# Optimization experiments

Measured on AMD Instinct MI355X. Metric: run time of the kernel, lower is better.

## Reference

```python
import jax, jax.numpy as jnp
import numpy as np

N_NODES = 100000
N_EDGES = 1600000
C = 64


def _spline_conv(x, src, dst, u, w, root, bias, n_nodes):
    """SplineConv, dim=1, kernel_size=2, degree=1, open spline, aggr='mean'.

    For K=2, degree=1, pseudo u in [0,1]: basis = (1-u) on knot 0, u on knot 1.
    message_e = (1-u_e) * x[src_e] @ w[0] + u_e * x[src_e] @ w[1]
    Compute the two GEMMs at node level (N < E) then gather, which is
    mathematically identical and cheaper.
    """
    h0 = x @ w[0]  # [N, C]
    h1 = x @ w[1]  # [N, C]
    uc = u[:, None]  # [E, 1]
    msg = (1.0 - uc) * h0[src] + uc * h1[src]  # [E, C]
    agg = jax.ops.segment_sum(msg, dst, num_segments=n_nodes)  # [N, C]
    deg = jax.ops.segment_sum(jnp.ones_like(u), dst, num_segments=n_nodes)
    agg = agg / jnp.maximum(deg, 1.0)[:, None]  # mean aggregation
    return agg + x @ root + bias


def setup_inputs() -> dict:
    key = jax.random.key(0)
    ks = jax.random.split(key, 10)
    x = jax.random.normal(ks[0], (N_NODES, C), dtype=jnp.float32)
    edge_index = jax.random.randint(ks[1], (2, N_EDGES), 0, N_NODES, dtype=jnp.int64)
    edge_attr = jax.random.uniform(ks[2], (N_EDGES, 1), dtype=jnp.float32)
    s = 1.0 / np.sqrt(C)
    w1 = jax.random.uniform(ks[3], (2, C, C), jnp.float32, -s, s)
    root1 = jax.random.uniform(ks[4], (C, C), jnp.float32, -s, s)
    b1 = jnp.zeros((C,), jnp.float32)
    w2 = jax.random.uniform(ks[5], (2, C, C), jnp.float32, -s, s)
    root2 = jax.random.uniform(ks[6], (C, C), jnp.float32, -s, s)
    b2 = jnp.zeros((C,), jnp.float32)
    return {"x": x, "edge_index": edge_index, "edge_attr": edge_attr,
            "w1": w1, "root1": root1, "b1": b1,
            "w2": w2, "root2": root2, "b2": b2}


def reference(x, edge_index, edge_attr, w1, root1, b1, w2, root2, b2):
    src, dst = edge_index[0], edge_index[1]
    u = edge_attr[:, 0]
    n = x.shape[0]
    h = _spline_conv(x, src, dst, u, w1, root1, b1, n)
    h = _spline_conv(h, src, dst, u, w2, root2, b2, n)
    return h
```

## Files before the change

### kernel.cpp

```cpp
#include <hip/hip_runtime.h>

#define CDIM 64

typedef __attribute__((ext_vector_type(8))) short bf16x8;
typedef __attribute__((ext_vector_type(4))) float f32x4;

__device__ __forceinline__ short bf16r(float f) {
    unsigned a = __float_as_uint(f);
    a = (a + 0x7fffu + ((a >> 16) & 1u)) >> 16;
    return (short)a;
}
__device__ __forceinline__ unsigned bfpack(float lo, float hi) {
    unsigned a = __float_as_uint(lo);
    a = (a + 0x7fffu + ((a >> 16) & 1u)) >> 16;
    unsigned b = __float_as_uint(hi);
    b = (b + 0x7fffu + ((b >> 16) & 1u)) & 0xffff0000u;
    return a | b;
}

#define NPB_SHIFT 9
#define BKN (1 << NPB_SHIFT)
#define BPAD 10240
#define PART_CH 2048
#define RCAP 1536

__global__ __launch_bounds__(256) void k_build(
        const int* __restrict__ src, const int* __restrict__ dst,
        const float* __restrict__ u, int* __restrict__ bkt_cursor,
        unsigned long long* __restrict__ rec, int n_edges, int n_buckets, int gP,
        const float* __restrict__ x, unsigned* __restrict__ xb32, size_t n2,
        const float* __restrict__ w1, const float* __restrict__ root1,
        const float* __restrict__ w2, const float* __restrict__ root2,
        short* __restrict__ wtg) {
    __shared__ int cnt_s[256];
    __shared__ int excl_s[256];
    __shared__ int cur_s[256];
    __shared__ int goff_s[256];
    __shared__ int tot_s;
    __shared__ unsigned long long rec_s[PART_CH];
    __shared__ int tgt_s[PART_CH];
    int tid = threadIdx.x;
    int bid = blockIdx.x;

    if (bid >= gP) {
        int r = bid - gP;
        if (r < 2) {
            const float* s0 = r ? w2 : w1;
            const float* srcs[3] = {s0, s0 + 4096, r ? root2 : root1};
            short* o = wtg + (size_t)r * 3 * 4096;
            for (int i = tid; i < 12288; i += 256) {
                int m = i >> 12, rr = i & 4095, k = rr >> 6, n = rr & 63;
                o[(m << 12) + (n << 6) + k] = bf16r(srcs[m][rr]);
            }
        } else {
            size_t t = (size_t)(r - 2) * 256 + tid;
            size_t stride = (size_t)(gridDim.x - gP - 2) * 256;
            for (size_t i = t; i < n2; i += stride) {
                float2 v = ((const float2*)x)[i];
                xb32[i] = bfpack(v.x, v.y);
            }
        }
        return;
    }

    cnt_s[tid] = 0;
    __syncthreads();
    int e0 = bid * PART_CH + tid * 8;
    int d[8], s[8];
    float uu[8];
    if (e0 + 8 <= n_edges) {
        int4 d0 = *(const int4*)(dst + e0), d1 = *(const int4*)(dst + e0 + 4);
        int4 s0 = *(const int4*)(src + e0), s1 = *(const int4*)(src + e0 + 4);
        float4 u0 = *(const float4*)(u + e0), u1 = *(const float4*)(u + e0 + 4);
        d[0]=d0.x; d[1]=d0.y; d[2]=d0.z; d[3]=d0.w; d[4]=d1.x; d[5]=d1.y; d[6]=d1.z; d[7]=d1.w;
        s[0]=s0.x; s[1]=s0.y; s[2]=s0.z; s[3]=s0.w; s[4]=s1.x; s[5]=s1.y; s[6]=s1.z; s[7]=s1.w;
        uu[0]=u0.x; uu[1]=u0.y; uu[2]=u0.z; uu[3]=u0.w; uu[4]=u1.x; uu[5]=u1.y; uu[6]=u1.z; uu[7]=u1.w;
    } else {
#pragma unroll
        for (int i = 0; i < 8; ++i) {
            int e = e0 + i;
            bool ok = e < n_edges;
            d[i] = ok ? dst[e] : -1;
            s[i] = ok ? src[e] : 0;
            uu[i] = ok ? u[e] : 0.f;
        }
    }
#pragma unroll
    for (int i = 0; i < 8; ++i)
        if (d[i] >= 0) atomicAdd(&cnt_s[d[i] >> NPB_SHIFT], 1);
    __syncthreads();
    int c = cnt_s[tid];
    excl_s[tid] = c;
    __syncthreads();
    for (int off = 1; off < 256; off <<= 1) {
        int t = (tid >= off) ? excl_s[tid - off] : 0;
        __syncthreads();
        excl_s[tid] += t;
        __syncthreads();
    }
    int excl = excl_s[tid] - c;
    if (tid == 255) tot_s = excl_s[255];
    __syncthreads();
    excl_s[tid] = excl;
    cur_s[tid] = excl;
    goff_s[tid] = 0;
    if (tid < n_buckets && c) goff_s[tid] = tid * BPAD + atomicAdd(&bkt_cursor[tid], c);
    __syncthreads();
#pragma unroll
    for (int i = 0; i < 8; ++i) {
        if (d[i] >= 0) {
            int b = d[i] >> NPB_SHIFT;
            int p = atomicAdd(&cur_s[b], 1);
            unsigned uq = (unsigned)(uu[i] * 32767.0f + 0.5f);
            rec_s[p] = ((unsigned long long)(unsigned)d[i] << 32)
                     | (unsigned long long)(((unsigned)s[i] << 15) | uq);
            tgt_s[p] = goff_s[b] + (p - excl_s[b]);
        }
    }
    __syncthreads();
    int tot = tot_s;
    for (int i = tid; i < tot; i += 256)
        rec[tgt_s[i]] = rec_s[i];
}

__global__ __launch_bounds__(512) void k_fused(
        const unsigned* __restrict__ xb_in,
        const unsigned long long* __restrict__ rec,
        const int* __restrict__ bkt_cursor,
        const short* __restrict__ wb,
        const float* __restrict__ bias,
        float* __restrict__ out,
        unsigned short* __restrict__ xb_out,
        unsigned* __restrict__ em_g,
        unsigned* __restrict__ rowcnt_g,
        int n_nodes, int n_buckets, int build) {
    __shared__ unsigned em_s[RCAP];
    __shared__ unsigned tmp_em[RCAP];
    __shared__ unsigned short tmp_d[RCAP];
    __shared__ int cnt_s[64];
    __shared__ int row_s[64];
    __shared__ int cur_s[64];
    __shared__ int nm_s;
    __shared__ __align__(16) unsigned gl[64][68];
    int tid = threadIdx.x;
    int blk = blockIdx.x;
    int b = (blk & 7) + 8 * (blk >> 6);
    int sub = (blk >> 3) & 7;
    if (b >= n_buckets) return;
    int lo = (b << NPB_SHIFT) + (sub << 6);
    int region = ((b << 3) + sub) * RCAP;
    const float inv15 = 1.0f / 32767.0f;

    if (build) {
        int nrec = bkt_cursor[b];
        const unsigned long long* r0 = rec + (size_t)b * BPAD;
        if (tid < 64) cnt_s[tid] = 0;
        if (tid == 0) nm_s = 0;
        __syncthreads();
        for (int i = tid; i < nrec; i += 512) {
            unsigned long long r = r0[i];
            int rel = (int)(r >> 32) - lo;
            if ((unsigned)rel < 64u) {
                int p = atomicAdd(&nm_s, 1);
                if (p < RCAP) {
                    tmp_em[p] = (unsigned)r;
                    tmp_d[p] = (unsigned short)rel;
                    atomicAdd(&cnt_s[rel], 1);
                }
            }
        }
        __syncthreads();
        if (tid < 64) row_s[tid] = cnt_s[tid];
        __syncthreads();
        for (int off = 1; off < 64; off <<= 1) {
            int t = (tid < 64 && tid >= off) ? row_s[tid - off] : 0;
            __syncthreads();
            if (tid < 64) row_s[tid] += t;
            __syncthreads();
        }
        if (tid < 64) {
            row_s[tid] -= cnt_s[tid];
            cur_s[tid] = row_s[tid];
        }
        __syncthreads();
        int nm = min(nm_s, RCAP);
        for (int i = tid; i < nm; i += 512) {
            int rel = tmp_d[i];
            int p = atomicAdd(&cur_s[rel], 1);
            em_s[p] = tmp_em[i];
        }
        __syncthreads();
        if (tid < 64)
            rowcnt_g[((b << 3) + sub) * 64 + tid] =
                (unsigned)row_s[tid] | ((unsigned)cnt_s[tid] << 16);
        for (int i = tid; i < nm; i += 512) em_g[region + i] = em_s[i];
    } else {
        if (tid < 64) {
            unsigned rc = rowcnt_g[((b << 3) + sub) * 64 + tid];
            row_s[tid] = (int)(rc & 0xffffu);
            cnt_s[tid] = (int)(rc >> 16);
        }
        __syncthreads();
    }

    const unsigned* em = build ? (const unsigned*)&em_s[0] : (em_g + region);
    int qid = tid >> 4;
    int ql = tid & 15;
    for (int t = 0; t < 2; ++t) {
        int rel = qid * 2 + t;
        int start = row_s[rel];
        int cnt = cnt_s[rel];
        int end = start + cnt;
        float a0 = 0.f, a1 = 0.f, a2 = 0.f, a3 = 0.f;
        float b0 = 0.f, b1 = 0.f, b2 = 0.f, b3 = 0.f;
        int j = start;
        for (; j + 4 <= end; j += 4) {
            unsigned e[4]; uint2 v[4];
#pragma unroll
            for (int i = 0; i < 4; ++i) e[i] = em[j + i];
#pragma unroll
            for (int i = 0; i < 4; ++i)
                v[i] = *(const uint2*)(xb_in + (size_t)(e[i] >> 15) * 32 + 2 * ql);
#pragma unroll
            for (int i = 0; i < 4; ++i) {
                float uu = (float)(e[i] & 0x7fffu) * inv15;
                float wa = 1.0f - uu;
                float c0 = __uint_as_float(v[i].x << 16);
                float c1 = __uint_as_float(v[i].x & 0xffff0000u);
                float c2 = __uint_as_float(v[i].y << 16);
                float c3 = __uint_as_float(v[i].y & 0xffff0000u);
                a0 += wa * c0; a1 += wa * c1; a2 += wa * c2; a3 += wa * c3;
                b0 += uu * c0; b1 += uu * c1; b2 += uu * c2; b3 += uu * c3;
            }
        }
        if (j < end) {
            unsigned e[4]; uint2 v[4]; float m[4];
#pragma unroll
            for (int i = 0; i < 4; ++i) {
                int idx = j + i;
                bool ok = idx < end;
                e[i] = em[ok ? idx : (end - 1)];
                m[i] = ok ? 1.0f : 0.0f;
            }
#pragma unroll
            for (int i = 0; i < 4; ++i)
                v[i] = *(const uint2*)(xb_in + (size_t)(e[i] >> 15) * 32 + 2 * ql);
#pragma unroll
            for (int i = 0; i < 4; ++i) {
                float uu = (float)(e[i] & 0x7fffu) * inv15;
                float wa = (1.0f - uu) * m[i], wu = uu * m[i];
                float c0 = __uint_as_float(v[i].x << 16);
                float c1 = __uint_as_float(v[i].x & 0xffff0000u);
                float c2 = __uint_as_float(v[i].y << 16);
                float c3 = __uint_as_float(v[i].y & 0xffff0000u);
                a0 += wa * c0; a1 += wa * c1; a2 += wa * c2; a3 += wa * c3;
                b0 += wu * c0; b1 += wu * c1; b2 += wu * c2; b3 += wu * c3;
            }
        }
        float s = 1.0f / fmaxf((float)cnt, 1.0f);
        *(uint2*)&gl[rel][2 * ql] = make_uint2(bfpack(a0 * s, a1 * s), bfpack(a2 * s, a3 * s));
        *(uint2*)&gl[rel][32 + 2 * ql] = make_uint2(bfpack(b0 * s, b1 * s), bfpack(b2 * s, b3 * s));
    }
    __syncthreads();

    int wv = tid >> 6;
    int lane = tid & 63;
    int tile = wv & 3;
    int nthalf = wv >> 2;
    int quad = lane >> 4;
    int m16 = lane & 15;
    int rown = tile * 16 + m16;
    int arow = lo + rown;
    bool rowok = arow < n_nodes;
    const short* gp = (const short*)&gl[rown][0];
    const unsigned* xp = xb_in + (size_t)arow * 32;
    bf16x8 zf = {0, 0, 0, 0, 0, 0, 0, 0};
    bf16x8 aG0[2], aG1[2], aX[2];
#pragma unroll
    for (int kf = 0; kf < 2; ++kf) {
        aG0[kf] = *(const bf16x8*)(gp + kf * 32 + quad * 8);
        aG1[kf] = *(const bf16x8*)(gp + 64 + kf * 32 + quad * 8);
        aX[kf] = rowok ? *(const bf16x8*)(xp + kf * 16 + quad * 4) : zf;
    }
#pragma unroll
    for (int nh = 0; nh < 2; ++nh) {
        int nt = nthalf * 2 + nh;
        f32x4 accv = {0.f, 0.f, 0.f, 0.f};
#pragma unroll
        for (int kf = 0; kf < 2; ++kf) {
            int col = nt * 16 + m16;
            bf16x8 bw0 = *(const bf16x8*)(wb + (col << 6) + kf * 32 + quad * 8);
            bf16x8 bw1 = *(const bf16x8*)(wb + ((64 + col) << 6) + kf * 32 + quad * 8);
            bf16x8 bwR = *(const bf16x8*)(wb + ((128 + col) << 6) + kf * 32 + quad * 8);
            accv = __builtin_amdgcn_mfma_f32_16x16x32_bf16(aG0[kf], bw0, accv, 0, 0, 0);
            accv = __builtin_amdgcn_mfma_f32_16x16x32_bf16(aG1[kf], bw1, accv, 0, 0, 0);
            accv = __builtin_amdgcn_mfma_f32_16x16x32_bf16(aX[kf], bwR, accv, 0, 0, 0);
        }
        float bcol = bias[nt * 16 + m16];
#pragma unroll
        for (int r = 0; r < 4; ++r) {
            int node = lo + tile * 16 + quad * 4 + r;
            if (node < n_nodes) {
                size_t off = (size_t)node * CDIM + nt * 16 + m16;
                float o = accv[r] + bcol;
                if (out) out[off] = o;
                if (xb_out) xb_out[off] = (unsigned short)bf16r(o);
            }
        }
    }
}

extern "C" void kernel_launch(void* const* d_in, const int* in_sizes, int n_in,
                              void* d_out, int out_size, void* d_ws, size_t ws_size,
                              hipStream_t stream) {
    const float* x = (const float*)d_in[0];
    const int* edge_index = (const int*)d_in[1];
    const float* edge_attr = (const float*)d_in[2];
    const float* w1 = (const float*)d_in[3];
    const float* root1 = (const float*)d_in[4];
    const float* b1 = (const float*)d_in[5];
    const float* w2 = (const float*)d_in[6];
    const float* root2 = (const float*)d_in[7];
    const float* b2 = (const float*)d_in[8];

    int n_nodes = in_sizes[0] / CDIM;
    int n_edges = in_sizes[2];
    const int* src = edge_index;
    const int* dst = edge_index + n_edges;

    size_t F = (size_t)n_nodes * CDIM;
    int n_buckets = (n_nodes + BKN - 1) >> NPB_SHIFT;
    int nb8 = n_buckets * 8;
    unsigned* xbA = (unsigned*)d_ws;
    unsigned* xbB = xbA + F / 2;
    int* bkt_cursor = (int*)(xbB + F / 2);
    uintptr_t p = (uintptr_t)(bkt_cursor + n_buckets);
    p = (p + 15) & ~(uintptr_t)15;
    short* wtg = (short*)p;
    p += (size_t)2 * 3 * 4096 * sizeof(short);
    p = (p + 15) & ~(uintptr_t)15;
    unsigned* em_g = (unsigned*)p;
    p += (size_t)nb8 * RCAP * sizeof(unsigned);
    unsigned* rowcnt_g = (unsigned*)p;
    p += (size_t)nb8 * 64 * sizeof(unsigned);
    p = (p + 15) & ~(uintptr_t)15;
    unsigned long long* rec = (unsigned long long*)p;
    float* out = (float*)d_out;

    int gP = (n_edges + PART_CH - 1) / PART_CH;
    int gB = gP + 2 + 2048;
    int gF = 64 * ((n_buckets + 7) / 8);

    hipMemsetAsync(bkt_cursor, 0, n_buckets * sizeof(int), stream);
    k_build<<<gB, 256, 0, stream>>>(src, dst, edge_attr, bkt_cursor, rec,
                                    n_edges, n_buckets, gP,
                                    x, xbA, F / 2, w1, root1, w2, root2, wtg);

    k_fused<<<gF, 512, 0, stream>>>(xbA, rec, bkt_cursor, wtg, b1,
                                    nullptr, (unsigned short*)xbB,
                                    em_g, rowcnt_g, n_nodes, n_buckets, 1);
    k_fused<<<gF, 512, 0, stream>>>(xbB, rec, bkt_cursor, wtg + 3 * 4096, b2,
                                    out, nullptr,
                                    em_g, rowcnt_g, n_nodes, n_buckets, 0);
}
```

Measured before the change: 257.7 us.

## Split fused kernel into specialized build and second-layer gather kernels

The single k_fused kernel is split into a build-specialized version for layer one and a lean k_go kernel for layer two. k_go uses 256-thread blocks with no build scratch in shared memory and only the 64x68 staging tile, so more blocks can be resident per CU during the gather-heavy second pass. It also uses a simpler linear block-to-node mapping. Bucket cursors are padded to separate cache lines to reduce atomic contention in k_build. The cost is extra code, and the padding makes the memset slightly larger.

Result: faster. 251.3 us (-2.5%).

```diff
diff --git a/kernel.cpp b/kernel.cpp
--- a/kernel.cpp
+++ b/kernel.cpp
@@ -23,6 +23,7 @@
 #define BPAD 10240
 #define PART_CH 2048
 #define RCAP 1536
+#define CPAD 16
 
 __global__ __launch_bounds__(256) void k_build(
         const int* __restrict__ src, const int* __restrict__ dst,
@@ -104,7 +105,8 @@
     excl_s[tid] = excl;
     cur_s[tid] = excl;
     goff_s[tid] = 0;
-    if (tid < n_buckets && c) goff_s[tid] = tid * BPAD + atomicAdd(&bkt_cursor[tid], c);
+    if (tid < n_buckets && c)
+        goff_s[tid] = tid * BPAD + atomicAdd(&bkt_cursor[tid * CPAD], c);
     __syncthreads();
 #pragma unroll
     for (int i = 0; i < 8; ++i) {
@@ -123,17 +125,16 @@
         rec[tgt_s[i]] = rec_s[i];
 }
 
-__global__ __launch_bounds__(512) void k_fused(
+__global__ __launch_bounds__(512) void k_fused_build(
         const unsigned* __restrict__ xb_in,
         const unsigned long long* __restrict__ rec,
         const int* __restrict__ bkt_cursor,
         const short* __restrict__ wb,
         const float* __restrict__ bias,
-        float* __restrict__ out,
         unsigned short* __restrict__ xb_out,
         unsigned* __restrict__ em_g,
         unsigned* __restrict__ rowcnt_g,
-        int n_nodes, int n_buckets, int build) {
+        int n_nodes, int n_buckets) {
     __shared__ unsigned em_s[RCAP];
     __shared__ unsigned tmp_em[RCAP];
     __shared__ unsigned short tmp_d[RCAP];
@@ -151,59 +152,49 @@
     int region = ((b << 3) + sub) * RCAP;
     const float inv15 = 1.0f / 32767.0f;
 
-    if (build) {
-        int nrec = bkt_cursor[b];
-        const unsigned long long* r0 = rec + (size_t)b * BPAD;
-        if (tid < 64) cnt_s[tid] = 0;
-        if (tid == 0) nm_s = 0;
+    int nrec = bkt_cursor[b * CPAD];
+    const unsigned long long* r0 = rec + (size_t)b * BPAD;
+    if (tid < 64) cnt_s[tid] = 0;
+    if (tid == 0) nm_s = 0;
+    __syncthreads();
+    for (int i = tid; i < nrec; i += 512) {
+        unsigned long long r = r0[i];
+        int rel = (int)(r >> 32) - lo;
+        if ((unsigned)rel < 64u) {
+            int p = atomicAdd(&nm_s, 1);
+            if (p < RCAP) {
+                tmp_em[p] = (unsigned)r;
+                tmp_d[p] = (unsigned short)rel;
+                atomicAdd(&cnt_s[rel], 1);
+            }
+        }
+    }
+    __syncthreads();
+    if (tid < 64) row_s[tid] = cnt_s[tid];
+    __syncthreads();
+    for (int off = 1; off < 64; off <<= 1) {
+        int t = (tid < 64 && tid >= off) ? row_s[tid - off] : 0;
         __syncthreads();
-        for (int i = tid; i < nrec; i += 512) {
-            unsigned long long r = r0[i];
-            int rel = (int)(r >> 32) - lo;
-            if ((unsigned)rel < 64u) {
-                int p = atomicAdd(&nm_s, 1);
-                if (p < RCAP) {
-                    tmp_em[p] = (unsigned)r;
-                    tmp_d[p] = (unsigned short)rel;
-                    atomicAdd(&cnt_s[rel], 1);
-                }
-            }
-        }
+        if (tid < 64) row_s[tid] += t;
         __syncthreads();
-        if (tid < 64) row_s[tid] = cnt_s[tid];
-        __syncthreads();
-        for (int off = 1; off < 64; off <<= 1) {
-            int t = (tid < 64 && tid >= off) ? row_s[tid - off] : 0;
-            __syncthreads();
-            if (tid < 64) row_s[tid] += t;
-            __syncthreads();
-        }
-        if (tid < 64) {
-            row_s[tid] -= cnt_s[tid];
-            cur_s[tid] = row_s[tid];
-        }
-        __syncthreads();
-        int nm = min(nm_s, RCAP);
-        for (int i = tid; i < nm; i += 512) {
-            int rel = tmp_d[i];
-            int p = atomicAdd(&cur_s[rel], 1);
-            em_s[p] = tmp_em[i];
-        }
-        __syncthreads();
-        if (tid < 64)
-            rowcnt_g[((b << 3) + sub) * 64 + tid] =
-                (unsigned)row_s[tid] | ((unsigned)cnt_s[tid] << 16);
-        for (int i = tid; i < nm; i += 512) em_g[region + i] = em_s[i];
-    } else {
-        if (tid < 64) {
-            unsigned rc = rowcnt_g[((b << 3) + sub) * 64 + tid];
-            row_s[tid] = (int)(rc & 0xffffu);
-            cnt_s[tid] = (int)(rc >> 16);
-        }
-        __syncthreads();
-    }
-
-    const unsigned* em = build ? (const unsigned*)&em_s[0] : (em_g + region);
+    }
+    if (tid < 64) {
+        row_s[tid] -= cnt_s[tid];
+        cur_s[tid] = row_s[tid];
+    }
+    __syncthreads();
+    int nm = min(nm_s, RCAP);
+    for (int i = tid; i < nm; i += 512) {
+        int rel = tmp_d[i];
+        int p = atomicAdd(&cur_s[rel], 1);
+        em_s[p] = tmp_em[i];
+    }
+    __syncthreads();
+    if (tid < 64)
+        rowcnt_g[((b << 3) + sub) * 64 + tid] =
+            (unsigned)row_s[tid] | ((unsigned)cnt_s[tid] << 16);
+    for (int i = tid; i < nm; i += 512) em_g[region + i] = em_s[i];
+
     int qid = tid >> 4;
     int ql = tid & 15;
     for (int t = 0; t < 2; ++t) {
@@ -217,7 +208,7 @@
         for (; j + 4 <= end; j += 4) {
             unsigned e[4]; uint2 v[4];
 #pragma unroll
-            for (int i = 0; i < 4; ++i) e[i] = em[j + i];
+            for (int i = 0; i < 4; ++i) e[i] = em_s[j + i];
 #pragma unroll
             for (int i = 0; i < 4; ++i)
                 v[i] = *(const uint2*)(xb_in + (size_t)(e[i] >> 15) * 32 + 2 * ql);
@@ -239,7 +230,7 @@
             for (int i = 0; i < 4; ++i) {
                 int idx = j + i;
                 bool ok = idx < end;
-                e[i] = em[ok ? idx : (end - 1)];
+                e[i] = em_s[ok ? idx : (end - 1)];
                 m[i] = ok ? 1.0f : 0.0f;
             }
 #pragma unroll
@@ -302,9 +293,123 @@
             int node = lo + tile * 16 + quad * 4 + r;
             if (node < n_nodes) {
                 size_t off = (size_t)node * CDIM + nt * 16 + m16;
-                float o = accv[r] + bcol;
-                if (out) out[off] = o;
-                if (xb_out) xb_out[off] = (unsigned short)bf16r(o);
+                xb_out[off] = (unsigned short)bf16r(accv[r] + bcol);
+            }
+        }
+    }
+}
+
+__global__ __launch_bounds__(256) void k_go(
+        const unsigned* __restrict__ xb_in,
+        const short* __restrict__ wb,
+        const float* __restrict__ bias,
+        float* __restrict__ out,
+        const unsigned* __restrict__ em_g,
+        const unsigned* __restrict__ rowcnt_g,
+        int n_nodes) {
+    __shared__ __align__(16) unsigned gl[64][68];
+    int tid = threadIdx.x;
+    int blk = blockIdx.x;
+    int wave = tid >> 6;
+    int lane = tid & 63;
+    int q = lane >> 4;
+    int ql = lane & 15;
+    int nodew = blk * 64 + wave * 16;
+    const unsigned* em = em_g + (size_t)blk * RCAP;
+    const unsigned* rc0 = rowcnt_g + (size_t)blk * 64;
+    const float inv15 = 1.0f / 32767.0f;
+
+    for (int t = 0; t < 4; ++t) {
+        int rel = wave * 16 + q * 4 + t;
+        unsigned rcv = rc0[rel];
+        int start = (int)(rcv & 0xffffu);
+        int cnt = (int)(rcv >> 16);
+        int end = start + cnt;
+        float a0 = 0.f, a1 = 0.f, a2 = 0.f, a3 = 0.f;
+        float b0 = 0.f, b1 = 0.f, b2 = 0.f, b3 = 0.f;
+        int j = start;
+        for (; j + 4 <= end; j += 4) {
+            unsigned e[4]; uint2 v[4];
+#pragma unroll
+            for (int i = 0; i < 4; ++i) e[i] = em[j + i];
+#pragma unroll
+            for (int i = 0; i < 4; ++i)
+                v[i] = *(const uint2*)(xb_in + (size_t)(e[i] >> 15) * 32 + 2 * ql);
+#pragma unroll
+            for (int i = 0; i < 4; ++i) {
+                float uu = (float)(e[i] & 0x7fffu) * inv15;
+                float wa = 1.0f - uu;
+                float c0 = __uint_as_float(v[i].x << 16);
+                float c1 = __uint_as_float(v[i].x & 0xffff0000u);
+                float c2 = __uint_as_float(v[i].y << 16);
+                float c3 = __uint_as_float(v[i].y & 0xffff0000u);
+                a0 += wa * c0; a1 += wa * c1; a2 += wa * c2; a3 += wa * c3;
+                b0 += uu * c0; b1 += uu * c1; b2 += uu * c2; b3 += uu * c3;
+            }
+        }
+        if (j < end) {
+            unsigned e[4]; uint2 v[4]; float m[4];
+#pragma unroll
+            for (int i = 0; i < 4; ++i) {
+                int idx = j + i;
+                bool ok = idx < end;
+                e[i] = em[ok ? idx : (end - 1)];
+                m[i] = ok ? 1.0f : 0.0f;
+            }
+#pragma unroll
+            for (int i = 0; i < 4; ++i)
+                v[i] = *(const uint2*)(xb_in + (size_t)(e[i] >> 15) * 32 + 2 * ql);
+#pragma unroll
+            for (int i = 0; i < 4; ++i) {
+                float uu = (float)(e[i] & 0x7fffu) * inv15;
+                float wa = (1.0f - uu) * m[i], wu = uu * m[i];
+                float c0 = __uint_as_float(v[i].x << 16);
+                float c1 = __uint_as_float(v[i].x & 0xffff0000u);
+                float c2 = __uint_as_float(v[i].y << 16);
+                float c3 = __uint_as_float(v[i].y & 0xffff0000u);
+                a0 += wa * c0; a1 += wa * c1; a2 += wa * c2; a3 += wa * c3;
+                b0 += wu * c0; b1 += wu * c1; b2 += wu * c2; b3 += wu * c3;
+            }
+        }
+        float s = 1.0f / fmaxf((float)cnt, 1.0f);
+        *(uint2*)&gl[rel][2 * ql] = make_uint2(bfpack(a0 * s, a1 * s), bfpack(a2 * s, a3 * s));
+        *(uint2*)&gl[rel][32 + 2 * ql] = make_uint2(bfpack(b0 * s, b1 * s), bfpack(b2 * s, b3 * s));
+    }
+
+    int quad = lane >> 4;
+    int m16 = lane & 15;
+    int arow = nodew + m16;
+    bool rowok = arow < n_nodes;
+    const short* gp = (const short*)&gl[wave * 16 + m16][0];
+    const unsigned* xp = xb_in + (size_t)arow * 32;
+    bf16x8 zf = {0, 0, 0, 0, 0, 0, 0, 0};
+    bf16x8 aG0[2], aG1[2], aX[2];
+#pragma unroll
+    for (int kf = 0; kf < 2; ++kf) {
+        aG0[kf] = *(const bf16x8*)(gp + kf * 32 + quad * 8);
+        aG1[kf] = *(const bf16x8*)(gp + 64 + kf * 32 + quad * 8);
+        aX[kf] = rowok ? *(const bf16x8*)(xp + kf * 16 + quad * 4) : zf;
+    }
+#pragma unroll
+    for (int nt = 0; nt < 4; ++nt) {
+        f32x4 accv = {0.f, 0.f, 0.f, 0.f};
+#pragma unroll
+        for (int kf = 0; kf < 2; ++kf) {
+            int col = nt * 16 + m16;
+            bf16x8 bw0 = *(const bf16x8*)(wb + (col << 6) + kf * 32 + quad * 8);
+            bf16x8 bw1 = *(const bf16x8*)(wb + ((64 + col) << 6) + kf * 32 + quad * 8);
+            bf16x8 bwR = *(const bf16x8*)(wb + ((128 + col) << 6) + kf * 32 + quad * 8);
+            accv = __builtin_amdgcn_mfma_f32_16x16x32_bf16(aG0[kf], bw0, accv, 0, 0, 0);
+            accv = __builtin_amdgcn_mfma_f32_16x16x32_bf16(aG1[kf], bw1, accv, 0, 0, 0);
+            accv = __builtin_amdgcn_mfma_f32_16x16x32_bf16(aX[kf], bwR, accv, 0, 0, 0);
+        }
+        float bcol = bias[nt * 16 + m16];
+#pragma unroll
+        for (int r = 0; r < 4; ++r) {
+            int node = nodew + quad * 4 + r;
+            if (node < n_nodes) {
+                size_t off = (size_t)node * CDIM + nt * 16 + m16;
+                out[off] = accv[r] + bcol;
             }
         }
     }
@@ -334,32 +439,32 @@
     unsigned* xbA = (unsigned*)d_ws;
     unsigned* xbB = xbA + F / 2;
     int* bkt_cursor = (int*)(xbB + F / 2);
-    uintptr_t p = (uintptr_t)(bkt_cursor + n_buckets);
-    p = (p + 15) & ~(uintptr_t)15;
+    uintptr_t p = (uintptr_t)(bkt_cursor + (size_t)n_buckets * CPAD);
+    p = (p + 63) & ~(uintptr_t)63;
     short* wtg = (short*)p;
     p += (size_t)2 * 3 * 4096 * sizeof(short);
-    p = (p + 15) & ~(uintptr_t)15;
+    p = (p + 63) & ~(uintptr_t)63;
     unsigned* em_g = (unsigned*)p;
     p += (size_t)nb8 * RCAP * sizeof(unsigned);
     unsigned* rowcnt_g = (unsigned*)p;
     p += (size_t)nb8 * 64 * sizeof(unsigned);
-    p = (p + 15) & ~(uintptr_t)15;
+    p = (p + 63) & ~(uintptr_t)63;
     unsigned long long* rec = (unsigned long long*)p;
     float* out = (float*)d_out;
 
     int gP = (n_edges + PART_CH - 1) / PART_CH;
     int gB = gP + 2 + 2048;
     int gF = 64 * ((n_buckets + 7) / 8);
-
-    hipMemsetAsync(bkt_cursor, 0, n_buckets * sizeof(int), stream);
+    int gG = (n_nodes + 63) / 64;
+
+    hipMemsetAsync(bkt_cursor, 0, (size_t)n_buckets * CPAD * sizeof(int), stream);
     k_build<<<gB, 256, 0, stream>>>(src, dst, edge_attr, bkt_cursor, rec,
                                     n_edges, n_buckets, gP,
                                     x, xbA, F / 2, w1, root1, w2, root2, wtg);
 
-    k_fused<<<gF, 512, 0, stream>>>(xbA, rec, bkt_cursor, wtg, b1,
-                                    nullptr, (unsigned short*)xbB,
-                                    em_g, rowcnt_g, n_nodes, n_buckets, 1);
-    k_fused<<<gF, 512, 0, stream>>>(xbB, rec, bkt_cursor, wtg + 3 * 4096, b2,
-                                    out, nullptr,
-                                    em_g, rowcnt_g, n_nodes, n_buckets, 0);
-}
+    k_fused_build<<<gF, 512, 0, stream>>>(xbA, rec, bkt_cursor, wtg, b1,
+                                          (unsigned short*)xbB,
+                                          em_g, rowcnt_g, n_nodes, n_buckets);
+    k_go<<<gG, 256, 0, stream>>>(xbB, wtg + 3 * 4096, b2, out,
+                                 em_g, rowcnt_g, n_nodes);
+}
```
